# Kernel tuning notes

Hardware: AMD Instinct MI355X
Metric: run time of the kernel (lower is better)

Reference implementation:

```python
import jax, jax.numpy as jnp
import numpy as np

B, L, H, D = 16, 2048, 768, 768
M, TPL = 8, 16  # labels per example, tokens per label


def setup_inputs() -> dict:
    key = jax.random.key(0)
    k1, k2, k3, k4 = jax.random.split(key, 4)
    hidden_states = jax.random.normal(k1, (B, L, H), dtype=jnp.float32)
    # first M*TPL tokens are label tokens with ids 1..M, rest are text tokens
    pos = jnp.arange(L)
    row = jnp.where(pos < M * TPL, pos // TPL + 1, 0).astype(jnp.int32)
    lmask = jnp.broadcast_to(row, (B, L))
    input_ids = jax.random.randint(k2, (B, L), 0, 30000, dtype=jnp.int32)
    attention_mask = jnp.ones((B, L), dtype=jnp.int32)
    Wt = jax.random.normal(k3, (H, D), dtype=jnp.float32) / np.sqrt(H)
    bt = jnp.zeros((D,), dtype=jnp.float32)
    Wl = jax.random.normal(k4, (H, D), dtype=jnp.float32) / np.sqrt(H)
    bl = jnp.zeros((D,), dtype=jnp.float32)
    attention_temperature = jnp.array(1.0, dtype=jnp.float32)
    logit_scale = jnp.array(2.0, dtype=jnp.float32)
    return dict(hidden_states=hidden_states, Wt=Wt, bt=bt, Wl=Wl, bl=bl,
                attention_temperature=attention_temperature, logit_scale=logit_scale,
                lmask=lmask, input_ids=input_ids, attention_mask=attention_mask,
                num_labels=M)


def reference(hidden_states, Wt, bt, Wl, bl, attention_temperature, logit_scale,
              lmask, input_ids, attention_mask, num_labels):
    # hidden_states: (B, L, H); lmask: (B, L) int label ids (>0 = label token)
    Bb, Ll, _ = hidden_states.shape
    Mm = num_labels  # static python int (== max label id)
    proj_text = hidden_states @ Wt + bt            # (B, L, D)  text_projector (dropout=eval identity)
    proj_label = hidden_states @ Wl + bl           # (B, L, D)  label_projector on all tokens
    label_tok = lmask > 0                          # (B, L)
    # segment-mean of projected label tokens per (batch, label_id) slot
    flat_idx = jnp.where(label_tok,
                         jnp.arange(Bb, dtype=lmask.dtype)[:, None] * Mm + (lmask - 1),
                         Bb * Mm).reshape(-1)
    masked = proj_label * label_tok[..., None].astype(proj_label.dtype)
    seg = jax.ops.segment_sum(masked.reshape(Bb * Ll, -1), flat_idx,
                              num_segments=Bb * Mm + 1)[: Bb * Mm]
    counts = jax.ops.segment_sum(label_tok.reshape(-1).astype(jnp.float32), flat_idx,
                                 num_segments=Bb * Mm + 1)[: Bb * Mm]
    aggregated_labels = seg / jnp.maximum(counts, 1.0)[:, None]   # (B*M, D)
    agg = aggregated_labels.reshape(Bb, Mm, -1)                   # (B, M, D)
    # attention-weighted text pooling per label over text tokens
    text_mask = (lmask == 0) & (attention_mask == 1)              # (B, L)
    temp = jnp.maximum(jnp.abs(attention_temperature), 0.1)
    scores = jnp.einsum('bmd,bld->bml', agg, proj_text) / temp
    scores = jnp.where(text_mask[:, None, :], scores, -jnp.inf)
    attn = jax.nn.softmax(scores, axis=-1)                        # (B, M, L)
    aggregated_text = jnp.einsum('bml,bld->bmd', attn, proj_text).reshape(Bb * Mm, -1)
    # cosine similarity head with learnable temperature exp(logit_scale)
    tn = aggregated_text / jnp.clip(jnp.linalg.norm(aggregated_text, axis=-1, keepdims=True), 1e-8)
    ln = aggregated_labels / jnp.clip(jnp.linalg.norm(aggregated_labels, axis=-1, keepdims=True), 1e-8)
    scale = jnp.exp(logit_scale)
    logits = jnp.sum(tn * ln, axis=-1, keepdims=True) * scale     # (B*M, 1)
    all_batch_ids = jnp.repeat(jnp.arange(Bb), Mm)
    all_label_ids = jnp.tile(jnp.arange(1, Mm + 1), Bb)
    return (logits, all_batch_ids, all_label_ids, aggregated_labels, scale, aggregated_text)
```

## Files before the change

### kernel.cpp

```cpp
#include <hip/hip_runtime.h>
#include <hip/hip_bf16.h>

typedef __attribute__((ext_vector_type(8))) short s16x8;
typedef __attribute__((ext_vector_type(4))) float f32x4;

#define BB 16
#define LL 2048
#define HH 768
#define DD 768
#define MM 8

#define O_LOGITS 0
#define O_BID    128
#define O_LID    256
#define O_AGGL   384
#define O_SCALE  98688
#define O_AGGT   98689

#define WTT_OFF  0u
#define WLT_OFF  1179648u
#define WTB_OFF  2359296u
#define HBAR_OFF 3538944u
#define QH_OFF   3932160u
#define HST_OFF  4325376u
#define CVEC_OFF 4718592u
#define PML_OFF  4719104u
#define PO_OFF   4751872u
#define SK_OFF   17334784u

__device__ __forceinline__ short f2bf(float x) {
  union { float f; unsigned u; } v; v.f = x;
  unsigned r = v.u + 0x7FFFu + ((v.u >> 16) & 1u);
  return (short)(r >> 16);
}

#define GLOAD_LDS16(gp, lp) __builtin_amdgcn_global_load_lds( \
    (const __attribute__((address_space(1))) unsigned int*)(gp), \
    (__attribute__((address_space(3))) unsigned int*)(lp), 16, 0, 0)

__global__ void k_prep(const float* __restrict__ Wt, const float* __restrict__ Wl,
                       short* __restrict__ Wtt, short* __restrict__ Wlt,
                       short* __restrict__ Wtb,
                       const float* __restrict__ hs, const int* __restrict__ lmask,
                       float* __restrict__ hbar) {
  __shared__ float tile[64][65];
  __shared__ int list[LL];
  __shared__ int nlist_s;
  int bx = blockIdx.x;
  int t = threadIdx.x;
  if (bx < 432) {
    int z = bx / 144, r = bx % 144;
    int kb = (r % 12) * 64, nb = (r / 12) * 64;
    int c = t & 63;
    int r0 = (t >> 6) * 16;
    if (z == 2) {
#pragma unroll
      for (int i = 0; i < 16; ++i) {
        int rr = kb + r0 + i;
        Wtb[(size_t)rr * DD + nb + c] = f2bf(Wt[(size_t)rr * DD + nb + c]);
      }
      return;
    }
    const float* src = z ? Wl : Wt;
    short* dst = z ? Wlt : Wtt;
#pragma unroll
    for (int i = 0; i < 16; ++i)
      tile[r0 + i][c] = src[(size_t)(kb + r0 + i) * DD + nb + c];
    __syncthreads();
#pragma unroll
    for (int i = 0; i < 16; ++i)
      dst[(size_t)(nb + r0 + i) * HH + kb + c] = f2bf(tile[c][r0 + i]);
    return;
  }
  int bh = bx - 432;
  int b = bh >> 3, m = bh & 7;
  int lane = t & 63, w = t >> 6;
  if (w == 0) {
    int base = 0;
    for (int win = 0; win < LL / 64; ++win) {
      int l = win * 64 + lane;
      bool match = (lmask[b * LL + l] == m + 1);
      unsigned long long mk = __ballot(match);
      if (match) {
        int pos = base + (int)__popcll(mk & ((1ull << lane) - 1ull));
        list[pos] = l;
      }
      base += (int)__popcll(mk);
    }
    if (lane == 0) nlist_s = base;
  }
  __syncthreads();
  int n = nlist_s;
  float inv = 1.0f / (float)(n > 1 ? n : 1);
  float a0 = 0.f, a1 = 0.f, a2 = 0.f;
  for (int i = 0; i < n; ++i) {
    const float* rr = hs + (size_t)(b * LL + list[i]) * HH;
    a0 += rr[t]; a1 += rr[t + 256]; a2 += rr[t + 512];
  }
  float* dst = hbar + (size_t)(b * MM + m) * HH;
  dst[t] = a0 * inv; dst[t + 256] = a1 * inv; dst[t + 512] = a2 * inv;
}

__global__ __launch_bounds__(256, 3)
void k_skgemm(const float* __restrict__ A, const short* __restrict__ Bt,
              float* __restrict__ part) {
  __shared__ short As[128][64];
  __shared__ short Bs[2][128][64];
  int t = threadIdx.x;
  int lane = t & 63, w = t >> 6;
  int wm = w >> 1, wn = w & 1;
  int n0 = blockIdx.x * 128;
  int kt0 = blockIdx.y * 3;

  f32x4 acc[4][4] = {};
  float4 areg[8];

  auto issueA = [&](int kt) {
    const float* Ag = A + (size_t)(kt0 + kt) * 64;
#pragma unroll
    for (int i = 0; i < 8; ++i) {
      int slot = i * 256 + t;
      int row = slot >> 4, c = slot & 15;
      areg[i] = *(const float4*)(Ag + (size_t)row * HH + c * 4);
    }
  };
  auto issueB = [&](int kt, int buf) {
    const short* Bg = Bt + (size_t)n0 * HH + (size_t)(kt0 + kt) * 64;
#pragma unroll
    for (int i = 0; i < 4; ++i) {
      int slot = i * 256 + w * 64 + lane;
      int row = slot >> 3, c = slot & 7;
      int cs = c ^ (row & 7);
      GLOAD_LDS16(Bg + (size_t)row * HH + cs * 8,
                  (char*)&Bs[0][0][0] + (size_t)buf * 16384 + (size_t)(i * 256 + w * 64) * 16);
    }
  };
  auto writeA = [&]() {
#pragma unroll
    for (int i = 0; i < 8; ++i) {
      int slot = i * 256 + t;
      int row = slot >> 4, c = slot & 15;
      unsigned d0, d1;
      asm("v_cvt_pk_bf16_f32 %0, %1, %2" : "=v"(d0) : "v"(areg[i].x), "v"(areg[i].y));
      asm("v_cvt_pk_bf16_f32 %0, %1, %2" : "=v"(d1) : "v"(areg[i].z), "v"(areg[i].w));
      int phys = (c >> 1) ^ (row & 7);
      uint2 val = {d0, d1};
      *(uint2*)((char*)&As[0][0] + (size_t)row * 128 + phys * 16 + (c & 1) * 8) = val;
    }
  };
  auto compute = [&](int buf) {
#pragma unroll
    for (int kk = 0; kk < 2; ++kk) {
      s16x8 a[4], bb[4];
#pragma unroll
      for (int i = 0; i < 4; ++i) {
        int row = wm * 64 + i * 16 + (lane & 15);
        int p = (kk * 4 + (lane >> 4)) ^ (row & 7);
        a[i] = *(const s16x8*)((const char*)&As[0][0] + (size_t)row * 128 + p * 16);
      }
#pragma unroll
      for (int i = 0; i < 4; ++i) {
        int row = wn * 64 + i * 16 + (lane & 15);
        int p = (kk * 4 + (lane >> 4)) ^ (row & 7);
        bb[i] = *(const s16x8*)((const char*)&Bs[0][0][0] + (size_t)buf * 16384 + (size_t)row * 128 + p * 16);
      }
#pragma unroll
      for (int mi = 0; mi < 4; ++mi)
#pragma unroll
        for (int ni = 0; ni < 4; ++ni)
          acc[mi][ni] = __builtin_amdgcn_mfma_f32_16x16x32_bf16(a[mi], bb[ni], acc[mi][ni], 0, 0, 0);
    }
  };

  issueA(0); issueB(0, 0);
  writeA();
  __syncthreads();
  for (int kt = 0; kt < 3; ++kt) {
    if (kt + 1 < 3) { issueA(kt + 1); issueB(kt + 1, (kt + 1) & 1); }
    compute(kt & 1);
    __syncthreads();
    if (kt + 1 < 3) {
      writeA();
      __syncthreads();
    }
  }

  float* po = part + (size_t)blockIdx.y * 128 * HH;
#pragma unroll
  for (int mi = 0; mi < 4; ++mi) {
    int row = wm * 64 + mi * 16 + ((lane >> 4) * 4);
#pragma unroll
    for (int ni = 0; ni < 4; ++ni) {
      int col = n0 + wn * 64 + ni * 16 + (lane & 15);
#pragma unroll
      for (int j = 0; j < 4; ++j)
        po[(size_t)(row + j) * HH + col] = acc[mi][ni][j];
    }
  }
}

__global__ void k_red_agg(const float* __restrict__ part, const float* __restrict__ bl,
                          const float* __restrict__ bt, float* __restrict__ out,
                          float* __restrict__ cvec) {
  int row = blockIdx.x;
  int t = threadIdx.x;
  int lane = t & 63, w = t >> 6;
  __shared__ float wred[4];
  float dotbt = 0.f;
#pragma unroll
  for (int cc = 0; cc < 3; ++cc) {
    int c = cc * 256 + t;
    float s = bl[c];
#pragma unroll
    for (int kc = 0; kc < 4; ++kc)
      s += part[((size_t)kc * 128 + row) * HH + c];
    out[O_AGGL + (size_t)row * DD + c] = s;
    dotbt += s * bt[c];
  }
  for (int sh = 32; sh; sh >>= 1) dotbt += __shfl_xor(dotbt, sh, 64);
  if (lane == 0) wred[w] = dotbt;
  __syncthreads();
  if (t == 0) cvec[row] = wred[0] + wred[1] + wred[2] + wred[3];
}

__global__ __launch_bounds__(512, 4)
void k_attnpool(const float* __restrict__ hs, const float* __restrict__ qhp,
                const float* __restrict__ cvec, const int* __restrict__ lmask,
                const int* __restrict__ amask, const float* __restrict__ temp_p,
                float* __restrict__ part_o, float* __restrict__ part_ml) {
  __shared__ short As[8][2][16][64];
  __shared__ short Bs[16][776];
  __shared__ float w_acc[4][64][4];
  __shared__ float w_lds[64][8];
  int chunk = blockIdx.x;
  int b = blockIdx.y;
  int t = threadIdx.x;
  int lane = t & 63, w = t >> 6;
  int wq = w & 3, kw = w >> 2;

  for (int c = t; c < HH; c += 512) {
#pragma unroll
    for (int r = 0; r < 8; ++r) {
      size_t o = (size_t)(b * MM + r) * HH + c;
      float s = qhp[o] + qhp[(size_t)128 * HH + o] + qhp[(size_t)256 * HH + o] + qhp[(size_t)384 * HH + o];
      Bs[r][c] = f2bf(s);
    }
#pragma unroll
    for (int r = 8; r < 16; ++r) Bs[r][c] = 0;
  }

  const float* Hg = hs + (size_t)(b * LL + chunk * 64) * HH;
  const float* Wrow = Hg + (size_t)(wq * 16) * HH;
  int kbase = kw * 384;
  float4 areg[2][4];

  auto issueA = [&](int set, int kt) {
#pragma unroll
    for (int i = 0; i < 4; ++i) {
      int slot = i * 64 + lane;
      int row = slot >> 4, c = slot & 15;
      if (set == 0)
        areg[0][i] = *(const float4*)(Wrow + (size_t)row * HH + kbase + kt * 64 + c * 4);
      else
        areg[1][i] = *(const float4*)(Wrow + (size_t)row * HH + kbase + kt * 64 + c * 4);
    }
  };
  auto writeA = [&](int set, int buf) {
#pragma unroll
    for (int i = 0; i < 4; ++i) {
      int slot = i * 64 + lane;
      int row = slot >> 4, c = slot & 15;
      float4 v = set == 0 ? areg[0][i] : areg[1][i];
      unsigned d0, d1;
      asm("v_cvt_pk_bf16_f32 %0, %1, %2" : "=v"(d0) : "v"(v.x), "v"(v.y));
      asm("v_cvt_pk_bf16_f32 %0, %1, %2" : "=v"(d1) : "v"(v.z), "v"(v.w));
      int phys = (c >> 1) ^ (row & 7);
      uint2 val = {d0, d1};
      *(uint2*)((char*)&As[w][buf][0][0] + (size_t)row * 128 + phys * 16 + (c & 1) * 8) = val;
    }
  };

  f32x4 acc = {};
  issueA(0, 0); issueA(1, 1);
  writeA(0, 0);
  __syncthreads();
#pragma unroll
  for (int kt = 0; kt < 6; ++kt) {
    int buf = kt & 1;
#pragma unroll
    for (int kk = 0; kk < 2; ++kk) {
      int r = lane & 15;
      int p = (kk * 4 + (lane >> 4)) ^ (r & 7);
      s16x8 a = *(const s16x8*)((const char*)&As[w][buf][0][0] + (size_t)r * 128 + p * 16);
      s16x8 bfr = *(const s16x8*)&Bs[lane & 15][kbase + kt * 64 + kk * 32 + (lane >> 4) * 8];
      acc = __builtin_amdgcn_mfma_f32_16x16x32_bf16(a, bfr, acc, 0, 0, 0);
    }
    if (kt + 1 < 6) writeA((kt + 1) & 1, (kt + 1) & 1);
    if (kt + 2 < 6) issueA(kt & 1, kt + 2);
  }

  if (kw == 1) {
    w_acc[wq][lane][0] = acc[0]; w_acc[wq][lane][1] = acc[1];
    w_acc[wq][lane][2] = acc[2]; w_acc[wq][lane][3] = acc[3];
  }
  __syncthreads();
  if (kw == 0) {
    acc[0] += w_acc[wq][lane][0]; acc[1] += w_acc[wq][lane][1];
    acc[2] += w_acc[wq][lane][2]; acc[3] += w_acc[wq][lane][3];
  }

  float inv_temp = 1.0f / fmaxf(fabsf(temp_p[0]), 0.1f);
  int m = lane & 15;
  int tok0 = wq * 16 + (lane >> 4) * 4;
  if (kw == 0 && m < MM) {
    float cv = cvec[b * MM + m];
    int4 lm = *(const int4*)&lmask[b * LL + chunk * 64 + tok0];
    int4 am = *(const int4*)&amask[b * LL + chunk * 64 + tok0];
    w_lds[tok0 + 0][m] = (lm.x == 0 && am.x == 1) ? (acc[0] + cv) * inv_temp : -1e30f;
    w_lds[tok0 + 1][m] = (lm.y == 0 && am.y == 1) ? (acc[1] + cv) * inv_temp : -1e30f;
    w_lds[tok0 + 2][m] = (lm.z == 0 && am.z == 1) ? (acc[2] + cv) * inv_temp : -1e30f;
    w_lds[tok0 + 3][m] = (lm.w == 0 && am.w == 1) ? (acc[3] + cv) * inv_temp : -1e30f;
  }
  __syncthreads();

  {
    float v = w_lds[lane][w];
    float mx = v;
    for (int s = 32; s; s >>= 1) mx = fmaxf(mx, __shfl_xor(mx, s, 64));
    float e = __expf(v - mx);
    float l = e;
    for (int s = 32; s; s >>= 1) l += __shfl_xor(l, s, 64);
    w_lds[lane][w] = e;
    if (lane == 0) {
      float* pml = part_ml + ((size_t)(chunk * BB + b) * MM + w) * 2;
      pml[0] = mx; pml[1] = l;
    }
  }
  __syncthreads();

  if (t < 384) {
    int h0 = t * 2;
    float2 o[8] = {};
    const float* hp = Hg + h0;
    for (int tok = 0; tok < 64; ++tok) {
      float2 hv = *(const float2*)(hp + (size_t)tok * HH);
      float4 w0 = *(const float4*)&w_lds[tok][0];
      float4 w1 = *(const float4*)&w_lds[tok][4];
      o[0].x += w0.x * hv.x; o[0].y += w0.x * hv.y;
      o[1].x += w0.y * hv.x; o[1].y += w0.y * hv.y;
      o[2].x += w0.z * hv.x; o[2].y += w0.z * hv.y;
      o[3].x += w0.w * hv.x; o[3].y += w0.w * hv.y;
      o[4].x += w1.x * hv.x; o[4].y += w1.x * hv.y;
      o[5].x += w1.y * hv.x; o[5].y += w1.y * hv.y;
      o[6].x += w1.z * hv.x; o[6].y += w1.z * hv.y;
      o[7].x += w1.w * hv.x; o[7].y += w1.w * hv.y;
    }
    float* po = part_o + (size_t)(chunk * BB + b) * MM * HH + h0;
#pragma unroll
    for (int mm = 0; mm < 8; ++mm)
      *(float2*)(po + (size_t)mm * HH) = o[mm];
  }
}

__global__ void k_finish(const float* __restrict__ part_o, const float* __restrict__ part_ml,
                         float* __restrict__ hst) {
  int row = blockIdx.x;
  int b = row >> 3, m = row & 7;
  int t = threadIdx.x;
  float mg = -1e30f;
#pragma unroll
  for (int lc = 0; lc < 32; ++lc)
    mg = fmaxf(mg, part_ml[((size_t)(lc * BB + b) * MM + m) * 2]);
  float L = 0.f;
  f32x4 acc = {};
  int h0 = t * 4;
  for (int lc = 0; lc < 32; ++lc) {
    const float* pml = part_ml + ((size_t)(lc * BB + b) * MM + m) * 2;
    float f = __expf(pml[0] - mg);
    L += pml[1] * f;
    f32x4 v = *(const f32x4*)(part_o + ((size_t)(lc * BB + b) * MM + m) * HH + h0);
    acc[0] += v[0] * f; acc[1] += v[1] * f; acc[2] += v[2] * f; acc[3] += v[3] * f;
  }
  float inv = 1.0f / L;
  f32x4 r = {acc[0] * inv, acc[1] * inv, acc[2] * inv, acc[3] * inv};
  *(f32x4*)(hst + (size_t)row * HH + h0) = r;
}

__global__ void k_head(const float* __restrict__ part, const float* __restrict__ bt,
                       const float* __restrict__ lscale_p, float* __restrict__ out) {
  int row = blockIdx.x;
  int lane = threadIdx.x;
  const float* al = out + O_AGGL + (size_t)row * DD;
  float dot = 0.f, nt = 0.f, nl = 0.f;
  for (int i = lane; i < DD; i += 64) {
    float a = bt[i];
#pragma unroll
    for (int kc = 0; kc < 4; ++kc)
      a += part[((size_t)kc * 128 + row) * HH + i];
    out[O_AGGT + (size_t)row * DD + i] = a;
    float c = al[i];
    dot += a * c; nt += a * a; nl += c * c;
  }
  for (int s = 32; s; s >>= 1) {
    dot += __shfl_xor(dot, s, 64);
    nt  += __shfl_xor(nt, s, 64);
    nl  += __shfl_xor(nl, s, 64);
  }
  if (lane == 0) {
    float scale = expf(lscale_p[0]);
    float denom = fmaxf(sqrtf(nt), 1e-8f) * fmaxf(sqrtf(nl), 1e-8f);
    out[O_LOGITS + row] = dot / denom * scale;
    out[O_BID + row] = (float)(row >> 3);
    out[O_LID + row] = (float)((row & 7) + 1);
    if (row == 0) out[O_SCALE] = scale;
  }
}

extern "C" void kernel_launch(void* const* d_in, const int* in_sizes, int n_in,
                              void* d_out, int out_size, void* d_ws, size_t ws_size,
                              hipStream_t stream) {
  const float* hs    = (const float*)d_in[0];
  const float* Wt    = (const float*)d_in[1];
  const float* bt    = (const float*)d_in[2];
  const float* Wl    = (const float*)d_in[3];
  const float* bl    = (const float*)d_in[4];
  const float* atemp = (const float*)d_in[5];
  const float* lsc   = (const float*)d_in[6];
  const int*   lmask = (const int*)d_in[7];
  const int*   amask = (const int*)d_in[9];
  float* out = (float*)d_out;
  char* ws = (char*)d_ws;
  short* Wtt  = (short*)(ws + WTT_OFF);
  short* Wlt  = (short*)(ws + WLT_OFF);
  short* Wtb  = (short*)(ws + WTB_OFF);
  float* hbar = (float*)(ws + HBAR_OFF);
  float* hst  = (float*)(ws + HST_OFF);
  float* cvec = (float*)(ws + CVEC_OFF);
  float* pml  = (float*)(ws + PML_OFF);
  float* po   = (float*)(ws + PO_OFF);
  float* skp  = (float*)(ws + SK_OFF);

  k_prep<<<560, 256, 0, stream>>>(Wt, Wl, Wtt, Wlt, Wtb, hs, lmask, hbar);
  k_skgemm<<<dim3(6, 4), 256, 0, stream>>>(hbar, Wlt, skp);
  k_red_agg<<<128, 256, 0, stream>>>(skp, bl, bt, out, cvec);
  k_skgemm<<<dim3(6, 4), 256, 0, stream>>>(out + O_AGGL, Wtb, skp);
  k_attnpool<<<dim3(32, 16), 512, 0, stream>>>(hs, skp, cvec, lmask, amask, atemp, po, pml);
  k_finish<<<128, 192, 0, stream>>>(po, pml, hst);
  k_skgemm<<<dim3(6, 4), 256, 0, stream>>>(hst, Wtt, skp);
  k_head<<<128, 64, 0, stream>>>(skp, bt, lsc, out);
}
```

Before: 84.47 us.

## Process 128 tokens per attnpool block and store partials in bf16

```diff
diff --git a/kernel.cpp b/kernel.cpp
--- a/kernel.cpp
+++ b/kernel.cpp
@@ -2,6 +2,7 @@
 #include <hip/hip_bf16.h>
 
 typedef __attribute__((ext_vector_type(8))) short s16x8;
+typedef __attribute__((ext_vector_type(4))) short s16x4;
 typedef __attribute__((ext_vector_type(4))) float f32x4;
 
 #define BB 16
@@ -9,6 +10,7 @@
 #define HH 768
 #define DD 768
 #define MM 8
+#define NCH 16
 
 #define O_LOGITS 0
 #define O_BID    128
@@ -21,7 +23,6 @@
 #define WLT_OFF  1179648u
 #define WTB_OFF  2359296u
 #define HBAR_OFF 3538944u
-#define QH_OFF   3932160u
 #define HST_OFF  4325376u
 #define CVEC_OFF 4718592u
 #define PML_OFF  4719104u
@@ -32,6 +33,10 @@
   union { float f; unsigned u; } v; v.f = x;
   unsigned r = v.u + 0x7FFFu + ((v.u >> 16) & 1u);
   return (short)(r >> 16);
+}
+__device__ __forceinline__ float bf2f(short x) {
+  union { unsigned u; float f; } v; v.u = ((unsigned)(unsigned short)x) << 16;
+  return v.f;
 }
 
 #define GLOAD_LDS16(gp, lp) __builtin_amdgcn_global_load_lds( \
@@ -223,15 +228,15 @@
   if (t == 0) cvec[row] = wred[0] + wred[1] + wred[2] + wred[3];
 }
 
-__global__ __launch_bounds__(512, 4)
+__global__ __launch_bounds__(512)
 void k_attnpool(const float* __restrict__ hs, const float* __restrict__ qhp,
                 const float* __restrict__ cvec, const int* __restrict__ lmask,
                 const int* __restrict__ amask, const float* __restrict__ temp_p,
-                float* __restrict__ part_o, float* __restrict__ part_ml) {
+                short* __restrict__ part_o, float* __restrict__ part_ml) {
   __shared__ short As[8][2][16][64];
   __shared__ short Bs[16][776];
   __shared__ float w_acc[4][64][4];
-  __shared__ float w_lds[64][8];
+  __shared__ float w_lds[128][8];
   int chunk = blockIdx.x;
   int b = blockIdx.y;
   int t = threadIdx.x;
@@ -249,88 +254,92 @@
     for (int r = 8; r < 16; ++r) Bs[r][c] = 0;
   }
 
-  const float* Hg = hs + (size_t)(b * LL + chunk * 64) * HH;
-  const float* Wrow = Hg + (size_t)(wq * 16) * HH;
+  const float* Hg = hs + (size_t)(b * LL + chunk * 128) * HH;
   int kbase = kw * 384;
+  float inv_temp = 1.0f / fmaxf(fabsf(temp_p[0]), 0.1f);
   float4 areg[2][4];
-
-  auto issueA = [&](int set, int kt) {
-#pragma unroll
-    for (int i = 0; i < 4; ++i) {
-      int slot = i * 64 + lane;
-      int row = slot >> 4, c = slot & 15;
-      if (set == 0)
-        areg[0][i] = *(const float4*)(Wrow + (size_t)row * HH + kbase + kt * 64 + c * 4);
-      else
-        areg[1][i] = *(const float4*)(Wrow + (size_t)row * HH + kbase + kt * 64 + c * 4);
-    }
-  };
-  auto writeA = [&](int set, int buf) {
-#pragma unroll
-    for (int i = 0; i < 4; ++i) {
-      int slot = i * 64 + lane;
-      int row = slot >> 4, c = slot & 15;
-      float4 v = set == 0 ? areg[0][i] : areg[1][i];
-      unsigned d0, d1;
-      asm("v_cvt_pk_bf16_f32 %0, %1, %2" : "=v"(d0) : "v"(v.x), "v"(v.y));
-      asm("v_cvt_pk_bf16_f32 %0, %1, %2" : "=v"(d1) : "v"(v.z), "v"(v.w));
-      int phys = (c >> 1) ^ (row & 7);
-      uint2 val = {d0, d1};
-      *(uint2*)((char*)&As[w][buf][0][0] + (size_t)row * 128 + phys * 16 + (c & 1) * 8) = val;
-    }
-  };
-
-  f32x4 acc = {};
-  issueA(0, 0); issueA(1, 1);
-  writeA(0, 0);
   __syncthreads();
-#pragma unroll
-  for (int kt = 0; kt < 6; ++kt) {
-    int buf = kt & 1;
-#pragma unroll
-    for (int kk = 0; kk < 2; ++kk) {
-      int r = lane & 15;
-      int p = (kk * 4 + (lane >> 4)) ^ (r & 7);
-      s16x8 a = *(const s16x8*)((const char*)&As[w][buf][0][0] + (size_t)r * 128 + p * 16);
-      s16x8 bfr = *(const s16x8*)&Bs[lane & 15][kbase + kt * 64 + kk * 32 + (lane >> 4) * 8];
-      acc = __builtin_amdgcn_mfma_f32_16x16x32_bf16(a, bfr, acc, 0, 0, 0);
-    }
-    if (kt + 1 < 6) writeA((kt + 1) & 1, (kt + 1) & 1);
-    if (kt + 2 < 6) issueA(kt & 1, kt + 2);
-  }
-
-  if (kw == 1) {
-    w_acc[wq][lane][0] = acc[0]; w_acc[wq][lane][1] = acc[1];
-    w_acc[wq][lane][2] = acc[2]; w_acc[wq][lane][3] = acc[3];
-  }
-  __syncthreads();
-  if (kw == 0) {
-    acc[0] += w_acc[wq][lane][0]; acc[1] += w_acc[wq][lane][1];
-    acc[2] += w_acc[wq][lane][2]; acc[3] += w_acc[wq][lane][3];
-  }
-
-  float inv_temp = 1.0f / fmaxf(fabsf(temp_p[0]), 0.1f);
-  int m = lane & 15;
-  int tok0 = wq * 16 + (lane >> 4) * 4;
-  if (kw == 0 && m < MM) {
-    float cv = cvec[b * MM + m];
-    int4 lm = *(const int4*)&lmask[b * LL + chunk * 64 + tok0];
-    int4 am = *(const int4*)&amask[b * LL + chunk * 64 + tok0];
-    w_lds[tok0 + 0][m] = (lm.x == 0 && am.x == 1) ? (acc[0] + cv) * inv_temp : -1e30f;
-    w_lds[tok0 + 1][m] = (lm.y == 0 && am.y == 1) ? (acc[1] + cv) * inv_temp : -1e30f;
-    w_lds[tok0 + 2][m] = (lm.z == 0 && am.z == 1) ? (acc[2] + cv) * inv_temp : -1e30f;
-    w_lds[tok0 + 3][m] = (lm.w == 0 && am.w == 1) ? (acc[3] + cv) * inv_temp : -1e30f;
-  }
-  __syncthreads();
+
+#pragma unroll
+  for (int st = 0; st < 2; ++st) {
+    const float* Wrow = Hg + (size_t)(st * 64 + wq * 16) * HH;
+
+    auto issueA = [&](int set, int kt) {
+#pragma unroll
+      for (int i = 0; i < 4; ++i) {
+        int slot = i * 64 + lane;
+        int row = slot >> 4, c = slot & 15;
+        if (set == 0)
+          areg[0][i] = *(const float4*)(Wrow + (size_t)row * HH + kbase + kt * 64 + c * 4);
+        else
+          areg[1][i] = *(const float4*)(Wrow + (size_t)row * HH + kbase + kt * 64 + c * 4);
+      }
+    };
+    auto writeA = [&](int set, int buf) {
+#pragma unroll
+      for (int i = 0; i < 4; ++i) {
+        int slot = i * 64 + lane;
+        int row = slot >> 4, c = slot & 15;
+        float4 v = set == 0 ? areg[0][i] : areg[1][i];
+        unsigned d0, d1;
+        asm("v_cvt_pk_bf16_f32 %0, %1, %2" : "=v"(d0) : "v"(v.x), "v"(v.y));
+        asm("v_cvt_pk_bf16_f32 %0, %1, %2" : "=v"(d1) : "v"(v.z), "v"(v.w));
+        int phys = (c >> 1) ^ (row & 7);
+        uint2 val = {d0, d1};
+        *(uint2*)((char*)&As[w][buf][0][0] + (size_t)row * 128 + phys * 16 + (c & 1) * 8) = val;
+      }
+    };
+
+    f32x4 acc = {};
+    issueA(0, 0); issueA(1, 1);
+    writeA(0, 0);
+#pragma unroll
+    for (int kt = 0; kt < 6; ++kt) {
+      int buf = kt & 1;
+#pragma unroll
+      for (int kk = 0; kk < 2; ++kk) {
+        int r = lane & 15;
+        int p = (kk * 4 + (lane >> 4)) ^ (r & 7);
+        s16x8 a = *(const s16x8*)((const char*)&As[w][buf][0][0] + (size_t)r * 128 + p * 16);
+        s16x8 bfr = *(const s16x8*)&Bs[lane & 15][kbase + kt * 64 + kk * 32 + (lane >> 4) * 8];
+        acc = __builtin_amdgcn_mfma_f32_16x16x32_bf16(a, bfr, acc, 0, 0, 0);
+      }
+      if (kt + 1 < 6) writeA((kt + 1) & 1, (kt + 1) & 1);
+      if (kt + 2 < 6) issueA(kt & 1, kt + 2);
+    }
+
+    if (kw == 1) {
+      w_acc[wq][lane][0] = acc[0]; w_acc[wq][lane][1] = acc[1];
+      w_acc[wq][lane][2] = acc[2]; w_acc[wq][lane][3] = acc[3];
+    }
+    __syncthreads();
+    if (kw == 0) {
+      acc[0] += w_acc[wq][lane][0]; acc[1] += w_acc[wq][lane][1];
+      acc[2] += w_acc[wq][lane][2]; acc[3] += w_acc[wq][lane][3];
+    }
+
+    int m = lane & 15;
+    int tok0 = st * 64 + wq * 16 + (lane >> 4) * 4;
+    if (kw == 0 && m < MM) {
+      float cv = cvec[b * MM + m];
+      int4 lm = *(const int4*)&lmask[b * LL + chunk * 128 + tok0];
+      int4 am = *(const int4*)&amask[b * LL + chunk * 128 + tok0];
+      w_lds[tok0 + 0][m] = (lm.x == 0 && am.x == 1) ? (acc[0] + cv) * inv_temp : -1e30f;
+      w_lds[tok0 + 1][m] = (lm.y == 0 && am.y == 1) ? (acc[1] + cv) * inv_temp : -1e30f;
+      w_lds[tok0 + 2][m] = (lm.z == 0 && am.z == 1) ? (acc[2] + cv) * inv_temp : -1e30f;
+      w_lds[tok0 + 3][m] = (lm.w == 0 && am.w == 1) ? (acc[3] + cv) * inv_temp : -1e30f;
+    }
+    __syncthreads();
+  }
 
   {
-    float v = w_lds[lane][w];
-    float mx = v;
+    float v0 = w_lds[lane][w], v1 = w_lds[64 + lane][w];
+    float mx = fmaxf(v0, v1);
     for (int s = 32; s; s >>= 1) mx = fmaxf(mx, __shfl_xor(mx, s, 64));
-    float e = __expf(v - mx);
-    float l = e;
+    float e0 = __expf(v0 - mx), e1 = __expf(v1 - mx);
+    float l = e0 + e1;
     for (int s = 32; s; s >>= 1) l += __shfl_xor(l, s, 64);
-    w_lds[lane][w] = e;
+    w_lds[lane][w] = e0; w_lds[64 + lane][w] = e1;
     if (lane == 0) {
       float* pml = part_ml + ((size_t)(chunk * BB + b) * MM + w) * 2;
       pml[0] = mx; pml[1] = l;
@@ -342,7 +351,7 @@
     int h0 = t * 2;
     float2 o[8] = {};
     const float* hp = Hg + h0;
-    for (int tok = 0; tok < 64; ++tok) {
+    for (int tok = 0; tok < 128; ++tok) {
       float2 hv = *(const float2*)(hp + (size_t)tok * HH);
       float4 w0 = *(const float4*)&w_lds[tok][0];
       float4 w1 = *(const float4*)&w_lds[tok][4];
@@ -355,31 +364,34 @@
       o[6].x += w1.z * hv.x; o[6].y += w1.z * hv.y;
       o[7].x += w1.w * hv.x; o[7].y += w1.w * hv.y;
     }
-    float* po = part_o + (size_t)(chunk * BB + b) * MM * HH + h0;
-#pragma unroll
-    for (int mm = 0; mm < 8; ++mm)
-      *(float2*)(po + (size_t)mm * HH) = o[mm];
-  }
-}
-
-__global__ void k_finish(const float* __restrict__ part_o, const float* __restrict__ part_ml,
+    short* po = part_o + (size_t)(chunk * BB + b) * MM * HH + h0;
+#pragma unroll
+    for (int mm = 0; mm < 8; ++mm) {
+      short2 pv = {f2bf(o[mm].x), f2bf(o[mm].y)};
+      *(short2*)(po + (size_t)mm * HH) = pv;
+    }
+  }
+}
+
+__global__ void k_finish(const short* __restrict__ part_o, const float* __restrict__ part_ml,
                          float* __restrict__ hst) {
   int row = blockIdx.x;
   int b = row >> 3, m = row & 7;
   int t = threadIdx.x;
   float mg = -1e30f;
 #pragma unroll
-  for (int lc = 0; lc < 32; ++lc)
+  for (int lc = 0; lc < NCH; ++lc)
     mg = fmaxf(mg, part_ml[((size_t)(lc * BB + b) * MM + m) * 2]);
   float L = 0.f;
   f32x4 acc = {};
   int h0 = t * 4;
-  for (int lc = 0; lc < 32; ++lc) {
+  for (int lc = 0; lc < NCH; ++lc) {
     const float* pml = part_ml + ((size_t)(lc * BB + b) * MM + m) * 2;
     float f = __expf(pml[0] - mg);
     L += pml[1] * f;
-    f32x4 v = *(const f32x4*)(part_o + ((size_t)(lc * BB + b) * MM + m) * HH + h0);
-    acc[0] += v[0] * f; acc[1] += v[1] * f; acc[2] += v[2] * f; acc[3] += v[3] * f;
+    s16x4 v = *(const s16x4*)(part_o + ((size_t)(lc * BB + b) * MM + m) * HH + h0);
+    acc[0] += bf2f(v[0]) * f; acc[1] += bf2f(v[1]) * f;
+    acc[2] += bf2f(v[2]) * f; acc[3] += bf2f(v[3]) * f;
   }
   float inv = 1.0f / L;
   f32x4 r = {acc[0] * inv, acc[1] * inv, acc[2] * inv, acc[3] * inv};
@@ -437,14 +449,14 @@
   float* hst  = (float*)(ws + HST_OFF);
   float* cvec = (float*)(ws + CVEC_OFF);
   float* pml  = (float*)(ws + PML_OFF);
-  float* po   = (float*)(ws + PO_OFF);
+  short* po   = (short*)(ws + PO_OFF);
   float* skp  = (float*)(ws + SK_OFF);
 
   k_prep<<<560, 256, 0, stream>>>(Wt, Wl, Wtt, Wlt, Wtb, hs, lmask, hbar);
   k_skgemm<<<dim3(6, 4), 256, 0, stream>>>(hbar, Wlt, skp);
   k_red_agg<<<128, 256, 0, stream>>>(skp, bl, bt, out, cvec);
   k_skgemm<<<dim3(6, 4), 256, 0, stream>>>(out + O_AGGL, Wtb, skp);
-  k_attnpool<<<dim3(32, 16), 512, 0, stream>>>(hs, skp, cvec, lmask, amask, atemp, po, pml);
+  k_attnpool<<<dim3(NCH, 16), 512, 0, stream>>>(hs, skp, cvec, lmask, amask, atemp, po, pml);
   k_finish<<<128, 192, 0, stream>>>(po, pml, hst);
   k_skgemm<<<dim3(6, 4), 256, 0, stream>>>(hst, Wtt, skp);
   k_head<<<128, 64, 0, stream>>>(skp, bt, lsc, out);
```

Result: no change. 84.28 us (-0.2%).
